# Optimization experiments

Hardware: AMD Instinct MI355X
Metric: run time of the kernel (lower is better)

Reference implementation:

```python
import jax, jax.numpy as jnp
import numpy as np

# dims: d=1024 model width, h=16 heads, d_head=64
B, S, D, H = 4, 1024, 1024, 16
RD = float(np.sqrt(D))
VAR_W_INIT = 0.001  # var_init[0]: initial weight-variance value


def setup_inputs() -> dict:
    key = jax.random.key(0)
    ks = jax.random.split(key, 5)
    x = jax.random.normal(ks[0], (B, S, D), jnp.float32)
    # input variance must be non-negative; small positive values
    var_x = jax.random.uniform(ks[1], (B, S, D), jnp.float32) * 0.01
    scale = 1.0 / np.sqrt(D)
    Wq = jax.random.normal(ks[2], (D, D), jnp.float32) * scale
    Wk = jax.random.normal(ks[3], (D, D), jnp.float32) * scale
    Wv = jax.random.normal(ks[4], (D, D), jnp.float32) * scale
    var_Wq = jnp.full((D, D), VAR_W_INIT, jnp.float32)
    var_Wk = jnp.full((D, D), VAR_W_INIT, jnp.float32)
    var_Wv = jnp.full((D, D), VAR_W_INIT, jnp.float32)
    return dict(x=x, var_x=var_x, Wq=Wq, var_Wq=var_Wq, Wk=Wk, var_Wk=var_Wk, Wv=Wv, var_Wv=var_Wv)


def _linear_vmp(x, var_x, W, var_W):
    # mean: x W^T ; variance of product of independent Gaussians:
    # var = var_x (W^2)^T + x^2 var_W^T + var_x var_W^T
    m = x @ W.T
    v = var_x @ (W * W).T + (x * x) @ var_W.T + var_x @ var_W.T
    return m, v


def _quadratic_vmp(m1, v1, m2, v2):
    # matmul of two independent Gaussian tensors (moment propagation)
    m = m1 @ m2
    v = v1 @ v2 + v1 @ (m2 * m2) + (m1 * m1) @ v2
    return m, v


def _softmax_vmp(a, var_a):
    # delta-method through softmax: J_ij = s_i(delta_ij - s_j)
    # var_i = s_i^2 [ (1-2 s_i) var_i + sum_j s_j^2 var_j ]
    s = jax.nn.softmax(a, axis=-1)
    sv = jnp.sum(s * s * var_a, axis=-1, keepdims=True)
    var_s = s * s * ((1.0 - 2.0 * s) * var_a + sv)
    return s, var_s


def _split_heads(t):
    b, s, _ = t.shape
    return t.reshape(b, s, H, D // H).transpose(0, 2, 1, 3)  # [B,H,S,dh]


def reference(x, var_x, Wq, var_Wq, Wk, var_Wk, Wv, var_Wv):
    q, vq = _linear_vmp(x, var_x, Wq, var_Wq)
    k, vk = _linear_vmp(x, var_x, Wk, var_Wk)
    v, vv = _linear_vmp(x, var_x, Wv, var_Wv)
    q, vq, k, vk, v, vv = map(_split_heads, (q, vq, k, vk, v, vv))
    kt = k.transpose(0, 1, 3, 2)
    vkt = vk.transpose(0, 1, 3, 2)
    a, va = _quadratic_vmp(q, vq, kt, vkt)          # [B,H,S,S]
    a, va = a / RD, va / (RD * RD)
    a, va = _softmax_vmp(a, va)                      # masking=False path
    o, vo = _quadratic_vmp(a, va, v, vv)             # [B,H,S,dh]
    o = o.transpose(0, 2, 1, 3).reshape(x.shape)
    vo = vo.transpose(0, 2, 1, 3).reshape(x.shape)
    # residual_vmp, mode='identity': mean add, variances add
    return x + o, var_x + vo
```

## Files before the change

### kernel.cpp

```cpp
#include <hip/hip_runtime.h>
#include <hip/hip_bf16.h>

#define BB 4
#define SS 1024
#define DD 1024
#define HH 16
#define DH 64
#define MM (BB*SS)

typedef __attribute__((ext_vector_type(8))) short bf16x8;
typedef __attribute__((ext_vector_type(8))) unsigned short u16x8;
typedef __attribute__((ext_vector_type(4))) float f32x4;

__device__ __forceinline__ float b2f(unsigned short u) {
    union { unsigned int i; float f; } c; c.i = ((unsigned int)u) << 16; return c.f;
}
__device__ __forceinline__ unsigned short f2b(float f) {
    __hip_bfloat16 h = __float2bfloat16(f);
    return *reinterpret_cast<unsigned short*>(&h);
}
__device__ __forceinline__ unsigned int pack2(float a, float b) {
    unsigned int r;
    asm("v_cvt_pk_bf16_f32 %0, %1, %2" : "=v"(r) : "v"(a), "v"(b));
    return r;
}
__device__ __forceinline__ void gload16(const unsigned short* g, unsigned short* l) {
    __builtin_amdgcn_global_load_lds(
        (const __attribute__((address_space(1))) void*)g,
        (__attribute__((address_space(3))) void*)l,
        16, 0, 0);
}
#define MFMA16(a, b, c) __builtin_amdgcn_mfma_f32_16x16x32_bf16(a, b, c, 0, 0, 0)

__global__ __launch_bounds__(256) void prep_x_kernel(
    const float* __restrict__ x, const float* __restrict__ vx,
    unsigned short* __restrict__ xb, unsigned short* __restrict__ vxb,
    unsigned short* __restrict__ xsb)
{
    const size_t i = ((size_t)blockIdx.x * 256 + threadIdx.x) * 4;
    float4 a = *(const float4*)(x + i);
    float4 b = *(const float4*)(vx + i);
    ushort4 oa = { f2b(a.x), f2b(a.y), f2b(a.z), f2b(a.w) };
    ushort4 ob = { f2b(b.x), f2b(b.y), f2b(b.z), f2b(b.w) };
    ushort4 os = { f2b(a.x*a.x), f2b(a.y*a.y), f2b(a.z*a.z), f2b(a.w*a.w) };
    *(ushort4*)(xb  + i) = oa;
    *(ushort4*)(vxb + i) = ob;
    *(ushort4*)(xsb + i) = os;
}

__global__ __launch_bounds__(256) void prep_w_kernel(
    const float* __restrict__ W0, const float* __restrict__ vW0,
    const float* __restrict__ W1, const float* __restrict__ vW1,
    const float* __restrict__ W2, const float* __restrict__ vW2,
    unsigned short* __restrict__ wp)
{
    const int z = blockIdx.y;
    const float* W  = (z==0)? W0 : (z==1)? W1 : W2;
    const float* vW = (z==0)? vW0: (z==1)? vW1: vW2;
    const size_t NW = (size_t)DD*DD;
    unsigned short* wb = wp + (size_t)(3*z+0)*NW;
    unsigned short* wc = wp + (size_t)(3*z+1)*NW;
    unsigned short* wv = wp + (size_t)(3*z+2)*NW;

    const size_t i = ((size_t)blockIdx.x * 256 + threadIdx.x) * 4;
    float4 a = *(const float4*)(W + i);
    float4 b = *(const float4*)(vW + i);
    ushort4 oa = { f2b(a.x), f2b(a.y), f2b(a.z), f2b(a.w) };
    ushort4 oc = { f2b(a.x*a.x + b.x), f2b(a.y*a.y + b.y),
                   f2b(a.z*a.z + b.z), f2b(a.w*a.w + b.w) };
    ushort4 ov = { f2b(b.x), f2b(b.y), f2b(b.z), f2b(b.w) };
    *(ushort4*)(wb + i) = oa;
    *(ushort4*)(wc + i) = oc;
    *(ushort4*)(wv + i) = ov;
}

__global__ __launch_bounds__(256) void gemm_proj_kernel(
    const unsigned short* __restrict__ xb, const unsigned short* __restrict__ vxb,
    const unsigned short* __restrict__ xsb,
    const unsigned short* __restrict__ wp,
    unsigned short* __restrict__ qm, unsigned short* __restrict__ km,
    unsigned short* __restrict__ vm,
    unsigned short* __restrict__ qv, unsigned short* __restrict__ kv,
    unsigned short* __restrict__ vvv)
{
    __shared__ unsigned short sA[2][128*32];
    __shared__ unsigned short sB[2][128*32];

    const int z = blockIdx.z;
    const size_t NW = (size_t)DD*DD;
    const bool isVar = (z >= 3);
    const int p = isVar ? (z - 3) : z;
    const unsigned short* A0 = isVar ? vxb : xb;
    const unsigned short* A1 = isVar ? xsb : xb;
    const unsigned short* B0 = wp + (size_t)(3*p + (isVar ? 1 : 0)) * NW;
    const unsigned short* B1 = isVar ? (wp + (size_t)(3*p + 2) * NW) : B0;
    unsigned short* Out = (z==0)? qm : (z==1)? km : (z==2)? vm
                        : (z==3)? qv : (z==4)? kv : vvv;
    const int NT = isVar ? 64 : 32;

    const int bn = blockIdx.x;
    const int bm = blockIdx.y;
    const int tid = threadIdx.x;
    const int w = tid >> 6;
    const int l = tid & 63;
    const int wr = w >> 1, wc = w & 1;

    const int r0 = tid >> 2;
    const int s0 = (((tid & 3) ^ ((r0 >> 1) & 3)) * 8);
    const size_t aoff0 = (size_t)(bm*128 + r0) * DD + s0;
    const size_t boff0 = (size_t)(bn*128 + r0) * DD + s0;
    const int ldsd0 = (w*64) * 8;
    const int ldsd1 = (256 + w*64) * 8;

#define STG(buf, t) do {                                                   \
        const unsigned short* As_ = ((t) < 32) ? A0 : A1;                  \
        const unsigned short* Bs_ = ((t) < 32) ? B0 : B1;                  \
        const int kc_ = ((t) & 31) * 32;                                   \
        gload16(As_ + aoff0 + kc_,                   &sA[buf][ldsd0]);     \
        gload16(As_ + aoff0 + (size_t)64*DD + kc_,   &sA[buf][ldsd1]);     \
        gload16(Bs_ + boff0 + kc_,                   &sB[buf][ldsd0]);     \
        gload16(Bs_ + boff0 + (size_t)64*DD + kc_,   &sB[buf][ldsd1]);     \
    } while (0)

    f32x4 acc[4][4];
    #pragma unroll
    for (int i = 0; i < 4; ++i)
        #pragma unroll
        for (int j = 0; j < 4; ++j)
            acc[i][j] = (f32x4){0.f,0.f,0.f,0.f};

    const int fr = l & 15;
    const int hi = l >> 4;

    STG(0, 0);
    __syncthreads();

    for (int t = 0; t < NT; ++t) {
        const int cb = t & 1;
        if (t + 1 < NT) STG(cb ^ 1, t + 1);

        bf16x8 bfr[4];
        #pragma unroll
        for (int j = 0; j < 4; ++j) {
            const int row = wc*64 + j*16 + fr;
            bfr[j] = *(const bf16x8*)&sB[cb][row*32 + ((hi ^ ((row >> 1) & 3)) * 8)];
        }
        #pragma unroll
        for (int i = 0; i < 4; ++i) {
            const int row = wr*64 + i*16 + fr;
            bf16x8 a0 = *(const bf16x8*)&sA[cb][row*32 + ((hi ^ ((row >> 1) & 3)) * 8)];
            #pragma unroll
            for (int j = 0; j < 4; ++j)
                acc[i][j] = MFMA16(a0, bfr[j], acc[i][j]);
        }
        __syncthreads();
    }
#undef STG

    const int orow = bm*128 + wr*64 + (hi << 2);
    const int ocol = bn*128 + wc*64 + fr;
    #pragma unroll
    for (int i = 0; i < 4; ++i)
        #pragma unroll
        for (int j = 0; j < 4; ++j)
            #pragma unroll
            for (int r = 0; r < 4; ++r)
                Out[(size_t)(orow + i*16 + r) * DD + ocol + j*16] = f2b(acc[i][j][r]);
}

__global__ __launch_bounds__(256) void prep_vt_kernel(
    const unsigned short* __restrict__ vm, const unsigned short* __restrict__ vvv,
    unsigned short* __restrict__ vt, unsigned short* __restrict__ wt,
    unsigned short* __restrict__ vvt)
{
    __shared__ unsigned short tv[64][68];
    __shared__ unsigned short tw[64][68];
    __shared__ unsigned short tvv[64][68];
    const int t = threadIdx.x;
    const int jt = blockIdx.x, h = blockIdx.y, b = blockIdx.z;
    const size_t ibase = (size_t)b*SS*DD + (size_t)h*DH;
    {
        const int j = t & 63, cg = t >> 6;
        const size_t ga = ibase + (size_t)(jt*64 + j)*DD + cg*16;
        #pragma unroll
        for (int hh = 0; hh < 2; ++hh) {
            u16x8 v8  = *(const u16x8*)(vm  + ga + hh*8);
            u16x8 vv8 = *(const u16x8*)(vvv + ga + hh*8);
            u16x8 w8;
            #pragma unroll
            for (int e = 0; e < 8; ++e) {
                float vf = b2f(v8[e]);
                w8[e] = f2b(b2f(vv8[e]) + vf*vf);
            }
            *(u16x8*)&tv[j][cg*16 + hh*8]  = v8;
            *(u16x8*)&tvv[j][cg*16 + hh*8] = vv8;
            *(u16x8*)&tw[j][cg*16 + hh*8]  = w8;
        }
    }
    __syncthreads();
    {
        const int d  = t >> 2;
        const int pc = t & 3;
        const int lc = pc ^ ((d >> 1) & 3);
        #pragma unroll
        for (int st = 0; st < 2; ++st) {
            u16x8 o0, o1, o2;
            #pragma unroll
            for (int e = 0; e < 8; ++e) {
                const int jl = st*32 + (e >> 2)*16 + lc*4 + (e & 3);
                o0[e] = tv[jl][d];
                o1[e] = tw[jl][d];
                o2[e] = tvv[jl][d];
            }
            const size_t ob = (size_t)((b*HH + h)*DH + d)*SS + jt*64 + st*32 + pc*8;
            *(u16x8*)(vt  + ob) = o0;
            *(u16x8*)(wt  + ob) = o1;
            *(u16x8*)(vvt + ob) = o2;
        }
    }
}

__global__ __launch_bounds__(256) void prep_kk_kernel(
    const unsigned short* __restrict__ kmp, const unsigned short* __restrict__ kvp,
    unsigned short* __restrict__ kkb)
{
    const size_t i = ((size_t)blockIdx.x * 256 + threadIdx.x) * 8;
    u16x8 k8 = *(const u16x8*)(kmp + i);
    u16x8 v8 = *(const u16x8*)(kvp + i);
    u16x8 o8;
    #pragma unroll
    for (int e = 0; e < 8; ++e) {
        float kf = b2f(k8[e]);
        o8[e] = f2b(b2f(v8[e]) + kf*kf);
    }
    *(u16x8*)(kkb + i) = o8;
}

union PW { unsigned int u[4]; bf16x8 v; };

__global__ __launch_bounds__(256, 3) void attn_mfma_kernel(
    const unsigned short* __restrict__ kmg, const unsigned short* __restrict__ kvg,
    const unsigned short* __restrict__ kkg,
    const unsigned short* __restrict__ vtg, const unsigned short* __restrict__ wtg,
    const unsigned short* __restrict__ vvtg,
    const unsigned short* __restrict__ qmg, const unsigned short* __restrict__ qvg,
    const float* __restrict__ x, const float* __restrict__ vx,
    float* __restrict__ om, float* __restrict__ ov)
{
    __shared__ unsigned short Ks[2][3][32*64];
    __shared__ unsigned short Vs[2][3][64*32];

    const int tid = threadIdx.x;
    const int w = tid >> 6, l = tid & 63;
    const int lo = l & 15, hi = l >> 4;

    const int fb = blockIdx.x;
    const int g  = ((fb >> 7) << 3) | (fb & 7);
    const int qt = (fb >> 3) & 15;
    const int h  = g & 15;
    const int b  = g >> 4;

    const size_t xbase = (size_t)b*SS*DD + (size_t)h*DH;
    const size_t vbase = (size_t)(b*HH + h)*DH*SS;

    bf16x8 qA[2], vqA[2], qsA[2];
    {
        const int qrow = qt*64 + w*16 + lo;
        #pragma unroll
        for (int ks = 0; ks < 2; ++ks) {
            const size_t ga = xbase + (size_t)qrow*DD + ks*32 + hi*8;
            qA[ks]  = *(const bf16x8*)(qmg + ga);
            vqA[ks] = *(const bf16x8*)(qvg + ga);
            #pragma unroll
            for (int e = 0; e < 8; ++e) {
                float f = b2f((unsigned short)qA[ks][e]);
                qsA[ks][e] = (short)f2b(f*f);
            }
        }
    }
    bf16x8 onesB;
    #pragma unroll
    for (int e = 0; e < 8; ++e) onesB[e] = (short)0x3F80;

    f32x4 T1[4], T2[4], T3[4], T4[4], T5[4];
    f32x4 zac = {0.f,0.f,0.f,0.f}, e2vac = {0.f,0.f,0.f,0.f};
    #pragma unroll
    for (int cb = 0; cb < 4; ++cb) {
        T1[cb] = (f32x4){0.f,0.f,0.f,0.f};
        T2[cb] = (f32x4){0.f,0.f,0.f,0.f};
        T3[cb] = (f32x4){0.f,0.f,0.f,0.f};
        T4[cb] = (f32x4){0.f,0.f,0.f,0.f};
        T5[cb] = (f32x4){0.f,0.f,0.f,0.f};
    }

    const size_t koff = (size_t)(l >> 3)*DD + (size_t)(((l & 7) ^ ((l >> 3) & 7)) * 8);
    const size_t voff = (size_t)(l >> 2)*SS + (size_t)((l & 3) * 8);

    const float KE = 0.03125f * 1.44269504f;

#define IK(bu, m, p, G) gload16(G + xbase + (j0 + (size_t)(p)*8)*DD + koff, &Ks[bu][m][(p)*512])
#define IV(bu, m, p, G) gload16(G + vbase + (size_t)((p)*16)*SS + j0 + voff, &Vs[bu][m][(p)*512])
#define STAGE(tt, bu) do {                                                     \
        const size_t j0 = (size_t)(tt) * 32;                                   \
        if (w == 0)      { IK(bu,0,0,kmg); IK(bu,0,1,kmg); IK(bu,0,2,kmg);     \
                           IK(bu,0,3,kmg); IK(bu,1,0,kvg); IK(bu,1,1,kvg); }   \
        else if (w == 1) { IK(bu,1,2,kvg); IK(bu,1,3,kvg); IK(bu,2,0,kkg);     \
                           IK(bu,2,1,kkg); IK(bu,2,2,kkg); IK(bu,2,3,kkg); }   \
        else if (w == 2) { IV(bu,0,0,vtg); IV(bu,0,1,vtg); IV(bu,0,2,vtg);     \
                           IV(bu,0,3,vtg); IV(bu,1,0,wtg); IV(bu,1,1,wtg); }   \
        else             { IV(bu,1,2,wtg); IV(bu,1,3,wtg); IV(bu,2,0,vvtg);    \
                           IV(bu,2,1,vvtg); IV(bu,2,2,vvtg); IV(bu,2,3,vvtg); }\
    } while (0)

    STAGE(0, 0);
    __syncthreads();

    int cur = 0;
    for (int t = 0; t < SS/32; ++t) {
        if (t + 1 < SS/32) STAGE(t + 1, cur ^ 1);

        PW pe, pe2, pev, pe3;
        #pragma unroll
        for (int jb = 0; jb < 2; ++jb) {
            f32x4 aa = {0.f,0.f,0.f,0.f}, vva = {0.f,0.f,0.f,0.f};
            const int jrow = jb*16 + lo;
            #pragma unroll
            for (int ks = 0; ks < 2; ++ks) {
                const int co = jrow*64 + (((ks*4 + hi) ^ (lo & 7)) * 8);
                bf16x8 kB  = *(const bf16x8*)&Ks[cur][0][co];
                bf16x8 vkB = *(const bf16x8*)&Ks[cur][1][co];
                bf16x8 kkB = *(const bf16x8*)&Ks[cur][2][co];
                aa  = MFMA16(kB,  qA[ks],  aa);
                vva = MFMA16(kkB, vqA[ks], vva);
                vva = MFMA16(vkB, qsA[ks], vva);
            }
            #pragma unroll
            for (int rp = 0; rp < 2; ++rp) {
                float e0 = exp2f(aa[rp*2]   * KE);
                float e1 = exp2f(aa[rp*2+1] * KE);
                float va0 = vva[rp*2], va1 = vva[rp*2+1];
                float s0 = e0*e0,  s1 = e1*e1;
                float v0 = s0*va0, v1 = s1*va1;
                float t0 = v0*e0,  t1 = v1*e1;
                pe.u [jb*2+rp] = pack2(e0, e1);
                pe2.u[jb*2+rp] = pack2(s0, s1);
                pev.u[jb*2+rp] = pack2(v0, v1);
                pe3.u[jb*2+rp] = pack2(t0, t1);
            }
        }

        __builtin_amdgcn_s_setprio(1);
        zac   = MFMA16(pe.v,  onesB, zac);
        e2vac = MFMA16(pev.v, onesB, e2vac);
        #pragma unroll
        for (int cb = 0; cb < 4; ++cb) {
            const int vo = (cb*16 + lo)*32 + ((hi ^ ((lo >> 1) & 3)) * 8);
            bf16x8 vB  = *(const bf16x8*)&Vs[cur][0][vo];
            bf16x8 wB  = *(const bf16x8*)&Vs[cur][1][vo];
            bf16x8 vvB = *(const bf16x8*)&Vs[cur][2][vo];
            T1[cb] = MFMA16(pe.v,  vB,  T1[cb]);
            T2[cb] = MFMA16(pev.v, wB,  T2[cb]);
            T3[cb] = MFMA16(pe3.v, wB,  T3[cb]);
            T4[cb] = MFMA16(pe2.v, wB,  T4[cb]);
            T5[cb] = MFMA16(pe2.v, vvB, T5[cb]);
        }
        __builtin_amdgcn_s_setprio(0);

        __syncthreads();
        cur ^= 1;
    }

    const float IRD2 = 0.0009765625f;
    #pragma unroll
    for (int r = 0; r < 4; ++r) {
        const float Z     = zac[r];
        const float invZ  = 1.f / Z;
        const float invZ2 = invZ * invZ;
        const float sv    = e2vac[r] * IRD2 * invZ2;
        const int row = qt*64 + w*16 + hi*4 + r;
        #pragma unroll
        for (int cb = 0; cb < 4; ++cb) {
            const size_t gi = xbase + (size_t)row*DD + cb*16 + lo;
            const float o  = T1[cb][r] * invZ;
            const float vo = (T2[cb][r]*IRD2 + sv*T4[cb][r] + T5[cb][r]) * invZ2
                           - 2.f * T3[cb][r] * IRD2 * invZ2 * invZ;
            om[gi] = x[gi] + o;
            ov[gi] = vx[gi] + vo;
        }
    }
#undef IK
#undef IV
#undef STAGE
}

extern "C" void kernel_launch(void* const* d_in, const int* in_sizes, int n_in,
                              void* d_out, int out_size, void* d_ws, size_t ws_size,
                              hipStream_t stream) {
    const float* x    = (const float*)d_in[0];
    const float* vx   = (const float*)d_in[1];
    const float* Wq   = (const float*)d_in[2];
    const float* vWq  = (const float*)d_in[3];
    const float* Wk   = (const float*)d_in[4];
    const float* vWk  = (const float*)d_in[5];
    const float* Wv   = (const float*)d_in[6];
    const float* vWv  = (const float*)d_in[7];

    const size_t NE = (size_t)MM * DD;
    const size_t NW = (size_t)DD * DD;

    unsigned short* u = (unsigned short*)d_ws;
    unsigned short* qm   = u + 0*NE;
    unsigned short* qv   = u + 1*NE;
    unsigned short* km   = u + 2*NE;
    unsigned short* kv   = u + 3*NE;
    unsigned short* vm   = u + 4*NE;
    unsigned short* vvv  = u + 5*NE;
    unsigned short* xbb  = u + 6*NE;
    unsigned short* vxbb = u + 7*NE;
    unsigned short* xsbb = u + 8*NE;
    unsigned short* wp   = u + 9*NE;

    float* om = (float*)d_out;
    float* ov = om + NE;

    prep_x_kernel<<<4096, 256, 0, stream>>>(x, vx, xbb, vxbb, xsbb);
    prep_w_kernel<<<dim3(1024, 3), 256, 0, stream>>>(Wq, vWq, Wk, vWk, Wv, vWv, wp);

    dim3 gg(8, 32, 6);
    gemm_proj_kernel<<<gg, 256, 0, stream>>>(xbb, vxbb, xsbb, wp,
                                             qm, km, vm, qv, kv, vvv);

    unsigned short* vt  = xbb;
    unsigned short* wt  = vxbb;
    unsigned short* vvt = xsbb;
    unsigned short* kkb = wp;
    dim3 gt(SS/64, HH, BB);
    prep_vt_kernel<<<gt, 256, 0, stream>>>(vm, vvv, vt, wt, vvt);
    prep_kk_kernel<<<2048, 256, 0, stream>>>(km, kv, kkb);

    attn_mfma_kernel<<<1024, 256, 0, stream>>>(km, kv, kkb, vt, wt, vvt,
                                               qm, qv, x, vx, om, ov);
}
```

Measured before the change: 202.6 us.

## Use 2 warps per attention block, each handling 32 query rows

The attention kernel now launches 128 threads per block instead of 256, and each wave processes two 16-row query sub-tiles, so every K/V fragment read from LDS feeds twice as many MFMAs. Loading of K and V tiles is split between the two waves. This cuts LDS read traffic per MFMA. In exchange, accumulator register use roughly doubles (launch bounds relaxed to 1), which lowers occupancy and gives fewer waves to hide global-load latency.

```diff
diff --git a/kernel.cpp b/kernel.cpp
--- a/kernel.cpp
+++ b/kernel.cpp
@@ -238,7 +238,7 @@
 
 union PW { unsigned int u[4]; bf16x8 v; };
 
-__global__ __launch_bounds__(256, 3) void attn_mfma_kernel(
+__global__ __launch_bounds__(128, 1) void attn_mfma_kernel(
     const unsigned short* __restrict__ kmg, const unsigned short* __restrict__ kvg,
     const unsigned short* __restrict__ kkg,
     const unsigned short* __restrict__ vtg, const unsigned short* __restrict__ wtg,
@@ -263,18 +263,19 @@
     const size_t xbase = (size_t)b*SS*DD + (size_t)h*DH;
     const size_t vbase = (size_t)(b*HH + h)*DH*SS;
 
-    bf16x8 qA[2], vqA[2], qsA[2];
-    {
-        const int qrow = qt*64 + w*16 + lo;
+    bf16x8 qA[2][2], vqA[2][2], qsA[2][2];
+    #pragma unroll
+    for (int qh = 0; qh < 2; ++qh) {
+        const int qrow = qt*64 + w*32 + qh*16 + lo;
         #pragma unroll
         for (int ks = 0; ks < 2; ++ks) {
             const size_t ga = xbase + (size_t)qrow*DD + ks*32 + hi*8;
-            qA[ks]  = *(const bf16x8*)(qmg + ga);
-            vqA[ks] = *(const bf16x8*)(qvg + ga);
+            qA[qh][ks]  = *(const bf16x8*)(qmg + ga);
+            vqA[qh][ks] = *(const bf16x8*)(qvg + ga);
             #pragma unroll
             for (int e = 0; e < 8; ++e) {
-                float f = b2f((unsigned short)qA[ks][e]);
-                qsA[ks][e] = (short)f2b(f*f);
+                float f = b2f((unsigned short)qA[qh][ks][e]);
+                qsA[qh][ks][e] = (short)f2b(f*f);
             }
         }
     }
@@ -282,15 +283,20 @@
     #pragma unroll
     for (int e = 0; e < 8; ++e) onesB[e] = (short)0x3F80;
 
-    f32x4 T1[4], T2[4], T3[4], T4[4], T5[4];
-    f32x4 zac = {0.f,0.f,0.f,0.f}, e2vac = {0.f,0.f,0.f,0.f};
-    #pragma unroll
-    for (int cb = 0; cb < 4; ++cb) {
-        T1[cb] = (f32x4){0.f,0.f,0.f,0.f};
-        T2[cb] = (f32x4){0.f,0.f,0.f,0.f};
-        T3[cb] = (f32x4){0.f,0.f,0.f,0.f};
-        T4[cb] = (f32x4){0.f,0.f,0.f,0.f};
-        T5[cb] = (f32x4){0.f,0.f,0.f,0.f};
+    f32x4 T1[4][2], T2[4][2], T3[4][2], T4[4][2], T5[4][2];
+    f32x4 zac[2], e2vac[2];
+    #pragma unroll
+    for (int qh = 0; qh < 2; ++qh) {
+        zac[qh]   = (f32x4){0.f,0.f,0.f,0.f};
+        e2vac[qh] = (f32x4){0.f,0.f,0.f,0.f};
+        #pragma unroll
+        for (int cb = 0; cb < 4; ++cb) {
+            T1[cb][qh] = (f32x4){0.f,0.f,0.f,0.f};
+            T2[cb][qh] = (f32x4){0.f,0.f,0.f,0.f};
+            T3[cb][qh] = (f32x4){0.f,0.f,0.f,0.f};
+            T4[cb][qh] = (f32x4){0.f,0.f,0.f,0.f};
+            T5[cb][qh] = (f32x4){0.f,0.f,0.f,0.f};
+        }
     }
 
     const size_t koff = (size_t)(l >> 3)*DD + (size_t)(((l & 7) ^ ((l >> 3) & 7)) * 8);
@@ -300,16 +306,17 @@
 
 #define IK(bu, m, p, G) gload16(G + xbase + (j0 + (size_t)(p)*8)*DD + koff, &Ks[bu][m][(p)*512])
 #define IV(bu, m, p, G) gload16(G + vbase + (size_t)((p)*16)*SS + j0 + voff, &Vs[bu][m][(p)*512])
-#define STAGE(tt, bu) do {                                                     \
-        const size_t j0 = (size_t)(tt) * 32;                                   \
-        if (w == 0)      { IK(bu,0,0,kmg); IK(bu,0,1,kmg); IK(bu,0,2,kmg);     \
-                           IK(bu,0,3,kmg); IK(bu,1,0,kvg); IK(bu,1,1,kvg); }   \
-        else if (w == 1) { IK(bu,1,2,kvg); IK(bu,1,3,kvg); IK(bu,2,0,kkg);     \
-                           IK(bu,2,1,kkg); IK(bu,2,2,kkg); IK(bu,2,3,kkg); }   \
-        else if (w == 2) { IV(bu,0,0,vtg); IV(bu,0,1,vtg); IV(bu,0,2,vtg);     \
-                           IV(bu,0,3,vtg); IV(bu,1,0,wtg); IV(bu,1,1,wtg); }   \
-        else             { IV(bu,1,2,wtg); IV(bu,1,3,wtg); IV(bu,2,0,vvtg);    \
-                           IV(bu,2,1,vvtg); IV(bu,2,2,vvtg); IV(bu,2,3,vvtg); }\
+#define STAGE(tt, bu) do {                                                       \
+        const size_t j0 = (size_t)(tt) * 32;                                     \
+        if (w == 0) {                                                            \
+            IK(bu,0,0,kmg); IK(bu,0,1,kmg); IK(bu,0,2,kmg); IK(bu,0,3,kmg);      \
+            IK(bu,1,0,kvg); IK(bu,1,1,kvg); IK(bu,1,2,kvg); IK(bu,1,3,kvg);      \
+            IK(bu,2,0,kkg); IK(bu,2,1,kkg); IK(bu,2,2,kkg); IK(bu,2,3,kkg);      \
+        } else {                                                                 \
+            IV(bu,0,0,vtg); IV(bu,0,1,vtg); IV(bu,0,2,vtg); IV(bu,0,3,vtg);      \
+            IV(bu,1,0,wtg); IV(bu,1,1,wtg); IV(bu,1,2,wtg); IV(bu,1,3,wtg);      \
+            IV(bu,2,0,vvtg); IV(bu,2,1,vvtg); IV(bu,2,2,vvtg); IV(bu,2,3,vvtg);  \
+        }                                                                        \
     } while (0)
 
     STAGE(0, 0);
@@ -319,10 +326,15 @@
     for (int t = 0; t < SS/32; ++t) {
         if (t + 1 < SS/32) STAGE(t + 1, cur ^ 1);
 
-        PW pe, pe2, pev, pe3;
+        PW pe[2], pe2[2], pev[2], pe3[2];
         #pragma unroll
         for (int jb = 0; jb < 2; ++jb) {
-            f32x4 aa = {0.f,0.f,0.f,0.f}, vva = {0.f,0.f,0.f,0.f};
+            f32x4 aa[2], vva[2];
+            #pragma unroll
+            for (int qh = 0; qh < 2; ++qh) {
+                aa[qh]  = (f32x4){0.f,0.f,0.f,0.f};
+                vva[qh] = (f32x4){0.f,0.f,0.f,0.f};
+            }
             const int jrow = jb*16 + lo;
             #pragma unroll
             for (int ks = 0; ks < 2; ++ks) {
@@ -330,39 +342,51 @@
                 bf16x8 kB  = *(const bf16x8*)&Ks[cur][0][co];
                 bf16x8 vkB = *(const bf16x8*)&Ks[cur][1][co];
                 bf16x8 kkB = *(const bf16x8*)&Ks[cur][2][co];
-                aa  = MFMA16(kB,  qA[ks],  aa);
-                vva = MFMA16(kkB, vqA[ks], vva);
-                vva = MFMA16(vkB, qsA[ks], vva);
-            }
-            #pragma unroll
-            for (int rp = 0; rp < 2; ++rp) {
-                float e0 = exp2f(aa[rp*2]   * KE);
-                float e1 = exp2f(aa[rp*2+1] * KE);
-                float va0 = vva[rp*2], va1 = vva[rp*2+1];
-                float s0 = e0*e0,  s1 = e1*e1;
-                float v0 = s0*va0, v1 = s1*va1;
-                float t0 = v0*e0,  t1 = v1*e1;
-                pe.u [jb*2+rp] = pack2(e0, e1);
-                pe2.u[jb*2+rp] = pack2(s0, s1);
-                pev.u[jb*2+rp] = pack2(v0, v1);
-                pe3.u[jb*2+rp] = pack2(t0, t1);
+                #pragma unroll
+                for (int qh = 0; qh < 2; ++qh) {
+                    aa[qh]  = MFMA16(kB,  qA[qh][ks],  aa[qh]);
+                    vva[qh] = MFMA16(kkB, vqA[qh][ks], vva[qh]);
+                    vva[qh] = MFMA16(vkB, qsA[qh][ks], vva[qh]);
+                }
+            }
+            #pragma unroll
+            for (int qh = 0; qh < 2; ++qh) {
+                #pragma unroll
+                for (int rp = 0; rp < 2; ++rp) {
+                    float e0 = exp2f(aa[qh][rp*2]   * KE);
+                    float e1 = exp2f(aa[qh][rp*2+1] * KE);
+                    float va0 = vva[qh][rp*2], va1 = vva[qh][rp*2+1];
+                    float s0 = e0*e0,  s1 = e1*e1;
+                    float v0 = s0*va0, v1 = s1*va1;
+                    float t0 = v0*e0,  t1 = v1*e1;
+                    pe [qh].u[jb*2+rp] = pack2(e0, e1);
+                    pe2[qh].u[jb*2+rp] = pack2(s0, s1);
+                    pev[qh].u[jb*2+rp] = pack2(v0, v1);
+                    pe3[qh].u[jb*2+rp] = pack2(t0, t1);
+                }
             }
         }
 
         __builtin_amdgcn_s_setprio(1);
-        zac   = MFMA16(pe.v,  onesB, zac);
-        e2vac = MFMA16(pev.v, onesB, e2vac);
+        #pragma unroll
+        for (int qh = 0; qh < 2; ++qh) {
+            zac[qh]   = MFMA16(pe[qh].v,  onesB, zac[qh]);
+            e2vac[qh] = MFMA16(pev[qh].v, onesB, e2vac[qh]);
+        }
         #pragma unroll
         for (int cb = 0; cb < 4; ++cb) {
             const int vo = (cb*16 + lo)*32 + ((hi ^ ((lo >> 1) & 3)) * 8);
             bf16x8 vB  = *(const bf16x8*)&Vs[cur][0][vo];
             bf16x8 wB  = *(const bf16x8*)&Vs[cur][1][vo];
             bf16x8 vvB = *(const bf16x8*)&Vs[cur][2][vo];
-            T1[cb] = MFMA16(pe.v,  vB,  T1[cb]);
-            T2[cb] = MFMA16(pev.v, wB,  T2[cb]);
-            T3[cb] = MFMA16(pe3.v, wB,  T3[cb]);
-            T4[cb] = MFMA16(pe2.v, wB,  T4[cb]);
-            T5[cb] = MFMA16(pe2.v, vvB, T5[cb]);
+            #pragma unroll
+            for (int qh = 0; qh < 2; ++qh) {
+                T1[cb][qh] = MFMA16(pe[qh].v,  vB,  T1[cb][qh]);
+                T2[cb][qh] = MFMA16(pev[qh].v, wB,  T2[cb][qh]);
+                T3[cb][qh] = MFMA16(pe3[qh].v, wB,  T3[cb][qh]);
+                T4[cb][qh] = MFMA16(pe2[qh].v, wB,  T4[cb][qh]);
+                T5[cb][qh] = MFMA16(pe2[qh].v, vvB, T5[cb][qh]);
+            }
         }
         __builtin_amdgcn_s_setprio(0);
 
@@ -372,20 +396,23 @@
 
     const float IRD2 = 0.0009765625f;
     #pragma unroll
-    for (int r = 0; r < 4; ++r) {
-        const float Z     = zac[r];
-        const float invZ  = 1.f / Z;
-        const float invZ2 = invZ * invZ;
-        const float sv    = e2vac[r] * IRD2 * invZ2;
-        const int row = qt*64 + w*16 + hi*4 + r;
-        #pragma unroll
-        for (int cb = 0; cb < 4; ++cb) {
-            const size_t gi = xbase + (size_t)row*DD + cb*16 + lo;
-            const float o  = T1[cb][r] * invZ;
-            const float vo = (T2[cb][r]*IRD2 + sv*T4[cb][r] + T5[cb][r]) * invZ2
-                           - 2.f * T3[cb][r] * IRD2 * invZ2 * invZ;
-            om[gi] = x[gi] + o;
-            ov[gi] = vx[gi] + vo;
+    for (int qh = 0; qh < 2; ++qh) {
+        #pragma unroll
+        for (int r = 0; r < 4; ++r) {
+            const float Z     = zac[qh][r];
+            const float invZ  = 1.f / Z;
+            const float invZ2 = invZ * invZ;
+            const float sv    = e2vac[qh][r] * IRD2 * invZ2;
+            const int row = qt*64 + w*32 + qh*16 + hi*4 + r;
+            #pragma unroll
+            for (int cb = 0; cb < 4; ++cb) {
+                const size_t gi = xbase + (size_t)row*DD + cb*16 + lo;
+                const float o  = T1[cb][qh][r] * invZ;
+                const float vo = (T2[cb][qh][r]*IRD2 + sv*T4[cb][qh][r] + T5[cb][qh][r]) * invZ2
+                               - 2.f * T3[cb][qh][r] * IRD2 * invZ2 * invZ;
+                om[gi] = x[gi] + o;
+                ov[gi] = vx[gi] + vo;
+            }
         }
     }
 #undef IK
@@ -438,6 +465,6 @@
     prep_vt_kernel<<<gt, 256, 0, stream>>>(vm, vvv, vt, wt, vvt);
     prep_kk_kernel<<<2048, 256, 0, stream>>>(km, kv, kkb);
 
-    attn_mfma_kernel<<<1024, 256, 0, stream>>>(km, kv, kkb, vt, wt, vvt,
+    attn_mfma_kernel<<<1024, 128, 0, stream>>>(km, kv, kkb, vt, wt, vvt,
                                                qm, qv, x, vx, om, ov);
 }
```

Result: slower. 219.3 us (+8.2%).
